# Performance work log

Measured on AMD Instinct MI355X. Metric: run time of the kernel, lower is better.

Reference implementation:

```python
import jax, jax.numpy as jnp
import numpy as np

VOCAB = 100000
EMBED = 300
HIDDEN = 300
BATCH = 32768
K_NEG = 10
N_CLASSES = 2
EPS = 1e-5
DENO_W = 1.0
CONO_W = 1.0


def setup_inputs() -> dict:
    key = jax.random.key(0)
    ks = jax.random.split(key, 12)
    init_range = 1.0 / EMBED
    return {
        "center_word_ids": jax.random.randint(ks[0], (BATCH,), 0, VOCAB),
        "context_word_ids": jax.random.randint(ks[1], (BATCH,), 0, VOCAB),
        "neg_context_ids": jax.random.randint(ks[2], (BATCH, K_NEG), 0, VOCAB),
        "party_label": jax.random.randint(ks[3], (BATCH,), 0, N_CLASSES),
        "center_emb": jax.random.uniform(ks[4], (VOCAB, EMBED), jnp.float32, -init_range, init_range),
        "context_emb": jax.random.normal(ks[5], (VOCAB, EMBED), jnp.float32) * 0.02,
        "W_enc": jax.random.normal(ks[6], (HIDDEN, EMBED), jnp.float32) * (1.0 / np.sqrt(EMBED)),
        "b_enc": jnp.zeros((HIDDEN,), jnp.float32),
        "W_dec": jax.random.normal(ks[7], (EMBED, HIDDEN), jnp.float32) * (1.0 / np.sqrt(HIDDEN)),
        "b_dec": jnp.zeros((EMBED,), jnp.float32),
        "W_cls": jax.random.normal(ks[8], (N_CLASSES, HIDDEN), jnp.float32) * (1.0 / np.sqrt(HIDDEN)),
        "b_cls": jnp.zeros((N_CLASSES,), jnp.float32),
    }


def reference(center_word_ids, context_word_ids, neg_context_ids, party_label,
              center_emb, context_emb, W_enc, b_enc, W_dec, b_dec, W_cls, b_cls):
    # encoder_forward (dropout p=0 -> identity)
    emb = center_emb[center_word_ids]                      # [B, E]
    enc = emb @ W_enc.T + b_enc                            # [B, H]
    # deno_forward: skip-gram negative sampling
    center_v = enc @ W_dec.T + b_dec                       # [B, E]
    ctx_v = context_emb[context_word_ids]                  # [B, E]
    pos_score = jnp.clip(jnp.sum(center_v * ctx_v, axis=1), -10.0, 10.0)
    pos = -jax.nn.log_sigmoid(pos_score)                   # [B]
    neg_v = context_emb[neg_context_ids]                   # [B, K, E]
    neg_score = jnp.clip(jnp.einsum('bke,be->bk', neg_v, center_v), -10.0, 10.0)
    neg = -jnp.sum(jax.nn.log_sigmoid(-neg_score), axis=1)  # [B]
    deno_loss = jnp.clip(jnp.mean(pos + neg), EPS, 10.0)
    # cono_forward + cross entropy
    logits = enc @ W_cls.T + b_cls                         # [B, C]
    logp = jax.nn.log_softmax(logits, axis=-1)
    nll = -jnp.take_along_axis(logp, party_label[:, None], axis=1)[:, 0]
    cono_loss = jnp.clip(jnp.mean(nll), EPS, 10.0)
    encoder_loss = jnp.clip(DENO_W * deno_loss + CONO_W * cono_loss, EPS, None)
    return jnp.stack([encoder_loss, deno_loss, cono_loss])
```

## Files before the change

### kernel.cpp

```cpp
#include <hip/hip_runtime.h>
#include <math.h>

#define VOCAB   100000
#define EMBED   300
#define HIDDEN  300
#define BATCH   32768
#define K_NEG   10
#define EPSV    1e-5f

#define KPAD      320
#define NPAD      384
#define CV_STRIDE 304
#define CTX8_STRIDE 304
#define FP8_SCALE 64.0f
#define FP8_DESCALE 0.015625f
#define NBUCKET 512

typedef __attribute__((ext_vector_type(8))) short  short8;
typedef __attribute__((ext_vector_type(4))) float  f32x4;
typedef __attribute__((ext_vector_type(2))) float  floatx2;

#if defined(__has_builtin)
#if __has_builtin(__builtin_amdgcn_cvt_pk_f32_fp8) && __has_builtin(__builtin_amdgcn_cvt_pk_fp8_f32)
#define HAVE_CVT_FP8 1
#endif
#endif

__device__ inline float b2f(unsigned short u) {
    union { unsigned int i; float f; } v; v.i = ((unsigned int)u) << 16; return v.f;
}
__device__ inline unsigned short f2b(float f) {
    union { float f; unsigned int i; } v; v.f = f;
    unsigned int r = v.i + 0x7FFFu + ((v.i >> 16) & 1u);
    return (unsigned short)(r >> 16);
}
__device__ inline void up2(unsigned int u, float& lo, float& hi) {
    union { unsigned int i; float f; } a, b;
    a.i = u << 16; b.i = u & 0xFFFF0000u;
    lo = a.f; hi = b.f;
}
__device__ inline float wave_red(float v) {
    #pragma unroll
    for (int o = 32; o; o >>= 1) v += __shfl_down(v, o);
    return v;
}
__device__ inline float softplusf(float x) {
    return x > 0.f ? x + log1pf(expf(-x)) : log1pf(expf(x));
}

__device__ inline float fp8_to_f(unsigned int u8) {
    const unsigned s = (u8 >> 7) & 1, e = (u8 >> 3) & 15, m = u8 & 7;
    float v;
    if (e) { union { unsigned i; float f; } b; b.i = ((e + 120u) << 23) | (m << 20); v = b.f; }
    else v = (float)m * 0.001953125f;
    return s ? -v : v;
}
__device__ inline unsigned char f_to_fp8(float x) {
    union { float f; unsigned i; } b; b.f = x;
    const unsigned s = (b.i >> 31) << 7;
    const float a = fabsf(x);
    if (a >= 440.f) return (unsigned char)(s | 0x7E);
    if (a < 0.015625f) {
        int m = (int)rintf(a * 512.f);
        return (unsigned char)(m >= 8 ? (s | 0x08) : (s | (unsigned)m));
    }
    unsigned r = (b.i & 0x7FFFFFFFu) + 0x7FFFFu + ((b.i >> 20) & 1u);
    unsigned e8 = (r >> 23) - 120u;
    unsigned m8 = (r >> 20) & 7u;
    if (e8 > 15u) return (unsigned char)(s | 0x7E);
    return (unsigned char)(s | (e8 << 3) | m8);
}
__device__ inline unsigned enc4fp8(float a, float b, float c, float d) {
#ifdef HAVE_CVT_FP8
    int v = 0;
    v = __builtin_amdgcn_cvt_pk_fp8_f32(a, b, v, false);
    v = __builtin_amdgcn_cvt_pk_fp8_f32(c, d, v, true);
    return (unsigned)v;
#else
    return (unsigned)f_to_fp8(a) | ((unsigned)f_to_fp8(b) << 8) |
           ((unsigned)f_to_fp8(c) << 16) | ((unsigned)f_to_fp8(d) << 24);
#endif
}
__device__ inline void dec4fp8(unsigned u, float* f) {
#ifdef HAVE_CVT_FP8
    floatx2 lo = __builtin_amdgcn_cvt_pk_f32_fp8((int)u, false);
    floatx2 hi = __builtin_amdgcn_cvt_pk_f32_fp8((int)u, true);
    f[0] = lo[0]; f[1] = lo[1]; f[2] = hi[0]; f[3] = hi[1];
#else
    f[0] = fp8_to_f(u); f[1] = fp8_to_f(u >> 8);
    f[2] = fp8_to_f(u >> 16); f[3] = fp8_to_f(u >> 24);
#endif
}

__device__ inline void load_lds16(const void* g, void* l) {
    __builtin_amdgcn_global_load_lds(
        (const __attribute__((address_space(1))) unsigned int*)g,
        (__attribute__((address_space(3))) unsigned int*)l, 16, 0, 0);
}

#define NW (2 * NPAD * 40)
#define NE (BATCH * 40)
#define NC (VOCAB * 19)

__global__ __launch_bounds__(256)
void prep_kernel(const float* __restrict__ W_enc, const float* __restrict__ W_dec,
                 const float* __restrict__ cemb, const int* __restrict__ cids,
                 const float* __restrict__ xemb,
                 unsigned short* __restrict__ wenc_b, unsigned short* __restrict__ wdec_b,
                 unsigned short* __restrict__ emb_b, unsigned char* __restrict__ ctx8)
{
    const int gid = blockIdx.x * 256 + threadIdx.x;
    if (gid < NW) {
        const int mat = gid / (NPAD * 40);
        const int rem = gid - mat * (NPAD * 40);
        const int r   = rem / 40;
        const int c8  = (rem - r * 40) * 8;
        const float* src = mat ? W_dec : W_enc;
        unsigned short* dst = mat ? wdec_b : wenc_b;
        unsigned short t[8];
        #pragma unroll
        for (int j = 0; j < 8; ++j) {
            const int c = c8 + j;
            t[j] = (r < 300 && c < 300) ? f2b(src[r * 300 + c]) : (unsigned short)0;
        }
        *(uint4*)(dst + (size_t)r * KPAD + c8) = *(const uint4*)t;
    } else if (gid < NW + NE) {
        const int g2  = gid - NW;
        const int row = g2 / 40;
        const int c8  = (g2 - row * 40) * 8;
        const float* src = cemb + (size_t)cids[row] * 300;
        unsigned short t[8];
        if (c8 + 7 < 300) {
            float4 a = *(const float4*)(src + c8);
            float4 b = *(const float4*)(src + c8 + 4);
            t[0]=f2b(a.x); t[1]=f2b(a.y); t[2]=f2b(a.z); t[3]=f2b(a.w);
            t[4]=f2b(b.x); t[5]=f2b(b.y); t[6]=f2b(b.z); t[7]=f2b(b.w);
        } else {
            #pragma unroll
            for (int j = 0; j < 8; ++j) {
                const int c = c8 + j;
                t[j] = (c < 300) ? f2b(src[c]) : (unsigned short)0;
            }
        }
        *(uint4*)(emb_b + (size_t)row * KPAD + c8) = *(const uint4*)t;
    } else if (gid < NW + NE + NC) {
        const int g3  = gid - (NW + NE);
        const int row = g3 / 19;
        const int l   = g3 - row * 19;
        const int e0  = l * 16;
        const float* src = xemb + (size_t)row * 300 + e0;
        float v[16];
        #pragma unroll
        for (int q = 0; q < 4; ++q) {
            if (e0 + q * 4 + 3 < 300) {
                float4 a = *(const float4*)(src + q * 4);
                v[q*4+0]=a.x; v[q*4+1]=a.y; v[q*4+2]=a.z; v[q*4+3]=a.w;
            } else {
                #pragma unroll
                for (int j = 0; j < 4; ++j) {
                    const int e = e0 + q * 4 + j;
                    v[q*4+j] = (e < 300) ? src[q*4+j] : 0.f;
                }
            }
        }
        unsigned u[4];
        #pragma unroll
        for (int q = 0; q < 4; ++q)
            u[q] = enc4fp8(v[q*4]*FP8_SCALE, v[q*4+1]*FP8_SCALE,
                           v[q*4+2]*FP8_SCALE, v[q*4+3]*FP8_SCALE);
        *(uint4*)(ctx8 + (size_t)row * CTX8_STRIDE + e0) = make_uint4(u[0],u[1],u[2],u[3]);
    }
}

template <int OSTRIDE, bool PAD_ZERO>
__global__ __launch_bounds__(256)
void mfma_gemm_kernel(const unsigned short* __restrict__ A,
                      const unsigned short* __restrict__ B,
                      const float* __restrict__ bias,
                      unsigned short* __restrict__ C)
{
    __shared__ unsigned short As[128 * 32];
    __shared__ unsigned short Bs[128 * 32];

    const int tid  = threadIdx.x;
    const int wave = tid >> 6;
    const int lane = tid & 63;
    const int m0 = blockIdx.y * 128;
    const int n0 = blockIdx.x * 128;

    const int wr = (wave & 1) * 64;
    const int wc = (wave >> 1) * 64;
    const int fr = lane & 15;
    const int fq = lane >> 4;

    const unsigned short* gA[2];
    const unsigned short* gB[2];
    int ldsOff[2];
    #pragma unroll
    for (int inst = 0; inst < 2; ++inst) {
        const int t = wave * 2 + inst;
        const int r = (t << 4) + (lane >> 2);
        const int c = ((lane & 3) - r - (r >> 2)) & 3;
        gA[inst] = A + (size_t)(m0 + r) * KPAD + c * 8;
        gB[inst] = B + (size_t)(n0 + r) * KPAD + c * 8;
        ldsOff[inst] = t << 9;
    }

    int aoff[4], boff[4];
    #pragma unroll
    for (int i = 0; i < 4; ++i) {
        const int ra = wr + i * 16 + fr;
        aoff[i] = (ra << 5) + (((fq + ra + (ra >> 2)) & 3) << 3);
        const int rb = wc + i * 16 + fr;
        boff[i] = (rb << 5) + (((fq + rb + (rb >> 2)) & 3) << 3);
    }

    f32x4 acc[4][4] = {};

    for (int k0 = 0; k0 < KPAD; k0 += 32) {
        #pragma unroll
        for (int inst = 0; inst < 2; ++inst) {
            load_lds16(gA[inst] + k0, As + ldsOff[inst]);
            load_lds16(gB[inst] + k0, Bs + ldsOff[inst]);
        }
        __syncthreads();

        short8 af[4], bf[4];
        #pragma unroll
        for (int i = 0; i < 4; ++i) af[i] = *(const short8*)&As[aoff[i]];
        #pragma unroll
        for (int j = 0; j < 4; ++j) bf[j] = *(const short8*)&Bs[boff[j]];
        __syncthreads();

        #pragma unroll
        for (int i = 0; i < 4; ++i)
            #pragma unroll
            for (int j = 0; j < 4; ++j)
                acc[i][j] = __builtin_amdgcn_mfma_f32_16x16x32_bf16(
                    af[i], bf[j], acc[i][j], 0, 0, 0);
    }

    #pragma unroll
    for (int i = 0; i < 4; ++i) {
        #pragma unroll
        for (int r = 0; r < 4; ++r) {
            const int m = m0 + wr + i * 16 + fq * 4 + r;
            unsigned short* crow = C + (size_t)m * OSTRIDE;
            #pragma unroll
            for (int j = 0; j < 4; ++j) {
                const int n = n0 + wc + j * 16 + fr;
                if (n < 300) {
                    crow[n] = f2b(acc[i][j][r] + bias[n]);
                } else if (PAD_ZERO && n < OSTRIDE) {
                    crow[n] = 0;
                }
            }
        }
    }
}

__global__ __launch_bounds__(256)
void score_ce_kernel(const unsigned short* __restrict__ cvb,
                     const unsigned short* __restrict__ encb,
                     const unsigned char* __restrict__ ctx8,
                     const int* __restrict__ ctx_ids, const int* __restrict__ neg_ids,
                     const int* __restrict__ labels,
                     const float* __restrict__ W_cls, const float* __restrict__ b_cls,
                     float* __restrict__ db, float* __restrict__ cb)
{
    const int g    = threadIdx.x >> 6;
    const int lane = threadIdx.x & 63;
    const int row  = blockIdx.x;
    const bool act = lane < 19;

    __shared__ float blk[2];
    if (threadIdx.x < 2) blk[threadIdx.x] = 0.f;
    __syncthreads();

    const uint4 Z4 = make_uint4(0, 0, 0, 0);

    if (g < 3) {
        int ids[4]; int nsc; bool hasPos = false;
        const int b = row * K_NEG;
        if (g == 0) {
            hasPos = true; nsc = 4;
            ids[0] = ctx_ids[row];
            ids[1] = neg_ids[b+0]; ids[2] = neg_ids[b+1]; ids[3] = neg_ids[b+2];
        } else if (g == 1) {
            nsc = 4;
            ids[0] = neg_ids[b+3]; ids[1] = neg_ids[b+4];
            ids[2] = neg_ids[b+5]; ids[3] = neg_ids[b+6];
        } else {
            nsc = 3;
            ids[0] = neg_ids[b+7]; ids[1] = neg_ids[b+8];
            ids[2] = neg_ids[b+9]; ids[3] = neg_ids[b+9];
        }

        const char* cvp = (const char*)(cvb + (size_t)row * CV_STRIDE);
        uint4 c0 = act ? *(const uint4*)(cvp + lane * 32)      : Z4;
        uint4 c1 = act ? *(const uint4*)(cvp + lane * 32 + 16) : Z4;

        uint4 gv[4];
        #pragma unroll
        for (int j = 0; j < 4; ++j)
            gv[j] = act ? *(const uint4*)(ctx8 + (size_t)ids[j] * CTX8_STRIDE + lane * 16)
                        : Z4;

        float cvf[16];
        up2(c0.x, cvf[0], cvf[1]);  up2(c0.y, cvf[2], cvf[3]);
        up2(c0.z, cvf[4], cvf[5]);  up2(c0.w, cvf[6], cvf[7]);
        up2(c1.x, cvf[8], cvf[9]);  up2(c1.y, cvf[10], cvf[11]);
        up2(c1.z, cvf[12], cvf[13]);up2(c1.w, cvf[14], cvf[15]);

        float ds[4];
        #pragma unroll
        for (int j = 0; j < 4; ++j) {
            float gf[16];
            dec4fp8(gv[j].x, gf); dec4fp8(gv[j].y, gf + 4);
            dec4fp8(gv[j].z, gf + 8); dec4fp8(gv[j].w, gf + 12);
            float s = 0.f;
            #pragma unroll
            for (int e = 0; e < 16; ++e) s = fmaf(cvf[e], gf[e], s);
            ds[j] = s;
        }
        #pragma unroll
        for (int j = 0; j < 4; ++j) ds[j] = wave_red(ds[j]);

        if (lane == 0) {
            float local = 0.f;
            #pragma unroll
            for (int j = 0; j < 4; ++j) {
                if (j < nsc) {
                    float s = fminf(10.f, fmaxf(-10.f, ds[j] * FP8_DESCALE));
                    local += softplusf((hasPos && j == 0) ? -s : s);
                }
            }
            atomicAdd(&blk[0], local);
        }
    } else {
        const char* evp = (const char*)(encb + (size_t)row * KPAD);
        uint4 e0 = act ? *(const uint4*)(evp + lane * 32)      : Z4;
        uint4 e1 = act ? *(const uint4*)(evp + lane * 32 + 16) : Z4;
        float ev[16];
        up2(e0.x, ev[0], ev[1]);  up2(e0.y, ev[2], ev[3]);
        up2(e0.z, ev[4], ev[5]);  up2(e0.w, ev[6], ev[7]);
        up2(e1.x, ev[8], ev[9]);  up2(e1.y, ev[10], ev[11]);
        up2(e1.z, ev[12], ev[13]);up2(e1.w, ev[14], ev[15]);

        float p0 = 0.f, p1 = 0.f;
        #pragma unroll
        for (int q = 0; q < 4; ++q) {
            const int e = lane * 16 + q * 4;
            if (e + 3 < 300) {
                float4 w0 = *(const float4*)(W_cls + e);
                float4 w1 = *(const float4*)(W_cls + 300 + e);
                p0 = fmaf(ev[q*4], w0.x, p0); p0 = fmaf(ev[q*4+1], w0.y, p0);
                p0 = fmaf(ev[q*4+2], w0.z, p0); p0 = fmaf(ev[q*4+3], w0.w, p0);
                p1 = fmaf(ev[q*4], w1.x, p1); p1 = fmaf(ev[q*4+1], w1.y, p1);
                p1 = fmaf(ev[q*4+2], w1.z, p1); p1 = fmaf(ev[q*4+3], w1.w, p1);
            } else {
                #pragma unroll
                for (int j = 0; j < 4; ++j) {
                    if (e + j < 300) {
                        p0 = fmaf(ev[q*4+j], W_cls[e + j], p0);
                        p1 = fmaf(ev[q*4+j], W_cls[300 + e + j], p1);
                    }
                }
            }
        }
        p0 = wave_red(p0); p1 = wave_red(p1);
        if (lane == 0) {
            const float l0 = p0 + b_cls[0];
            const float l1 = p1 + b_cls[1];
            const float mx = fmaxf(l0, l1);
            const float lse = mx + logf(expf(l0 - mx) + expf(l1 - mx));
            blk[1] = lse - (labels[row] ? l1 : l0);
        }
    }
    __syncthreads();
    if (threadIdx.x == 0) atomicAdd(&db[blockIdx.x & (NBUCKET - 1)], blk[0]);
    if (threadIdx.x == 1) atomicAdd(&cb[blockIdx.x & (NBUCKET - 1)], blk[1]);
}

__global__ __launch_bounds__(256)
void finalize_kernel(const float* __restrict__ db, const float* __restrict__ cb,
                     float* __restrict__ out)
{
    const int t = threadIdx.x;
    float d = db[t] + db[t + 256];
    float c = cb[t] + cb[t + 256];
    d = wave_red(d); c = wave_red(c);
    __shared__ float sd[4], sc[4];
    if ((t & 63) == 0) { sd[t >> 6] = d; sc[t >> 6] = c; }
    __syncthreads();
    if (t == 0) {
        const float inv = 1.0f / (float)BATCH;
        float deno = (sd[0] + sd[1] + sd[2] + sd[3]) * inv;
        float cono = (sc[0] + sc[1] + sc[2] + sc[3]) * inv;
        deno = fminf(10.f, fmaxf(EPSV, deno));
        cono = fminf(10.f, fmaxf(EPSV, cono));
        out[0] = fmaxf(EPSV, deno + cono);
        out[1] = deno;
        out[2] = cono;
    }
}

extern "C" void kernel_launch(void* const* d_in, const int* in_sizes, int n_in,
                              void* d_out, int out_size, void* d_ws, size_t ws_size,
                              hipStream_t stream)
{
    const int*   cids  = (const int*)d_in[0];
    const int*   ctx   = (const int*)d_in[1];
    const int*   neg   = (const int*)d_in[2];
    const int*   lab   = (const int*)d_in[3];
    const float* cemb  = (const float*)d_in[4];
    const float* xemb  = (const float*)d_in[5];
    const float* W_enc = (const float*)d_in[6];
    const float* b_enc = (const float*)d_in[7];
    const float* W_dec = (const float*)d_in[8];
    const float* b_dec = (const float*)d_in[9];
    const float* W_cls = (const float*)d_in[10];
    const float* b_cls = (const float*)d_in[11];
    float* out = (float*)d_out;

    unsigned short* emb_b  = (unsigned short*)d_ws;
    unsigned short* wenc_b = emb_b  + (size_t)BATCH * KPAD;
    unsigned short* wdec_b = wenc_b + (size_t)NPAD * KPAD;
    unsigned short* enc_b  = wdec_b + (size_t)NPAD * KPAD;
    unsigned short* cv_b   = enc_b  + (size_t)BATCH * KPAD;
    unsigned char*  ctx8   = (unsigned char*)(cv_b + (size_t)BATCH * CV_STRIDE);
    float* buckets = (float*)(ctx8 + (size_t)VOCAB * CTX8_STRIDE);
    float* db = buckets;
    float* cb = buckets + NBUCKET;

    hipMemsetAsync(buckets, 0, 2 * NBUCKET * sizeof(float), stream);

    const int nprep = (NW + NE + NC + 255) / 256;
    prep_kernel<<<nprep, 256, 0, stream>>>(W_enc, W_dec, cemb, cids, xemb,
                                           wenc_b, wdec_b, emb_b, ctx8);

    dim3 ggrid(3, BATCH / 128);
    mfma_gemm_kernel<KPAD, true><<<ggrid, 256, 0, stream>>>(emb_b, wenc_b, b_enc, enc_b);
    mfma_gemm_kernel<CV_STRIDE, true><<<ggrid, 256, 0, stream>>>(enc_b, wdec_b, b_dec, cv_b);

    score_ce_kernel<<<BATCH, 256, 0, stream>>>(cv_b, enc_b, ctx8, ctx, neg, lab,
                                               W_cls, b_cls, db, cb);
    finalize_kernel<<<1, 256, 0, stream>>>(db, cb, out);
}
```

Before: 426.3 us.

## Fold encoder and decoder into one weight and split score/CE kernels

After: 422.6 us. About the same (-0.9%).

```diff
diff --git a/kernel.cpp b/kernel.cpp
--- a/kernel.cpp
+++ b/kernel.cpp
@@ -12,6 +12,7 @@
 #define NPAD      384
 #define CV_STRIDE 304
 #define CTX8_STRIDE 304
+#define WC2_STRIDE 304
 #define FP8_SCALE 64.0f
 #define FP8_DESCALE 0.015625f
 #define NBUCKET 512
@@ -38,11 +39,6 @@
     union { unsigned int i; float f; } a, b;
     a.i = u << 16; b.i = u & 0xFFFF0000u;
     lo = a.f; hi = b.f;
-}
-__device__ inline float wave_red(float v) {
-    #pragma unroll
-    for (int o = 32; o; o >>= 1) v += __shfl_down(v, o);
-    return v;
 }
 __device__ inline float softplusf(float x) {
     return x > 0.f ? x + log1pf(expf(-x)) : log1pf(expf(x));
@@ -98,36 +94,18 @@
         (__attribute__((address_space(3))) unsigned int*)l, 16, 0, 0);
 }
 
-#define NW (2 * NPAD * 40)
 #define NE (BATCH * 40)
 #define NC (VOCAB * 19)
 
 __global__ __launch_bounds__(256)
-void prep_kernel(const float* __restrict__ W_enc, const float* __restrict__ W_dec,
-                 const float* __restrict__ cemb, const int* __restrict__ cids,
+void prep_kernel(const float* __restrict__ cemb, const int* __restrict__ cids,
                  const float* __restrict__ xemb,
-                 unsigned short* __restrict__ wenc_b, unsigned short* __restrict__ wdec_b,
                  unsigned short* __restrict__ emb_b, unsigned char* __restrict__ ctx8)
 {
     const int gid = blockIdx.x * 256 + threadIdx.x;
-    if (gid < NW) {
-        const int mat = gid / (NPAD * 40);
-        const int rem = gid - mat * (NPAD * 40);
-        const int r   = rem / 40;
-        const int c8  = (rem - r * 40) * 8;
-        const float* src = mat ? W_dec : W_enc;
-        unsigned short* dst = mat ? wdec_b : wenc_b;
-        unsigned short t[8];
-        #pragma unroll
-        for (int j = 0; j < 8; ++j) {
-            const int c = c8 + j;
-            t[j] = (r < 300 && c < 300) ? f2b(src[r * 300 + c]) : (unsigned short)0;
-        }
-        *(uint4*)(dst + (size_t)r * KPAD + c8) = *(const uint4*)t;
-    } else if (gid < NW + NE) {
-        const int g2  = gid - NW;
-        const int row = g2 / 40;
-        const int c8  = (g2 - row * 40) * 8;
+    if (gid < NE) {
+        const int row = gid / 40;
+        const int c8  = (gid - row * 40) * 8;
         const float* src = cemb + (size_t)cids[row] * 300;
         unsigned short t[8];
         if (c8 + 7 < 300) {
@@ -143,8 +121,8 @@
             }
         }
         *(uint4*)(emb_b + (size_t)row * KPAD + c8) = *(const uint4*)t;
-    } else if (gid < NW + NE + NC) {
-        const int g3  = gid - (NW + NE);
+    } else if (gid < NE + NC) {
+        const int g3  = gid - NE;
         const int row = g3 / 19;
         const int l   = g3 - row * 19;
         const int e0  = l * 16;
@@ -172,15 +150,84 @@
     }
 }
 
-template <int OSTRIDE, bool PAD_ZERO>
 __global__ __launch_bounds__(256)
-void mfma_gemm_kernel(const unsigned short* __restrict__ A,
-                      const unsigned short* __restrict__ B,
-                      const float* __restrict__ bias,
-                      unsigned short* __restrict__ C)
-{
-    __shared__ unsigned short As[128 * 32];
-    __shared__ unsigned short Bs[128 * 32];
+void w2_kernel(const float* __restrict__ Wd, const float* __restrict__ We,
+               unsigned short* __restrict__ w2p)
+{
+    __shared__ float ds[16][33];
+    __shared__ float es[32][17];
+    const int tid = threadIdx.x;
+    const int tn = tid >> 4, tk = tid & 15;
+    const int n = blockIdx.y * 16 + tn;
+    const int k = blockIdx.x * 16 + tk;
+
+    float acc = 0.f;
+    for (int h0 = 0; h0 < 300; h0 += 32) {
+        {
+            const int i = tid * 2;
+            const int a = i >> 5, h = i & 31;
+            const int rr = blockIdx.y * 16 + a;
+            #pragma unroll
+            for (int j = 0; j < 2; ++j) {
+                const int hh = h + j;
+                ds[a][hh] = (rr < 300 && h0 + hh < 300) ? Wd[rr * 300 + h0 + hh] : 0.f;
+            }
+        }
+        {
+            const int i = tid * 2;
+            const int h = i >> 4, c = i & 15;
+            const int cc = blockIdx.x * 16 + c;
+            #pragma unroll
+            for (int j = 0; j < 2; ++j)
+                es[h][c + j] = (h0 + h < 300 && cc + j < 300) ? We[(h0 + h) * 300 + cc + j] : 0.f;
+        }
+        __syncthreads();
+        #pragma unroll
+        for (int h = 0; h < 32; ++h)
+            acc = fmaf(ds[tn][h], es[h][tk], acc);
+        __syncthreads();
+    }
+    if (n < NPAD && k < KPAD)
+        w2p[n * KPAD + k] = (n < 300 && k < 300) ? f2b(acc) : (unsigned short)0;
+}
+
+__global__ __launch_bounds__(320)
+void wb_kernel(const float* __restrict__ Wd, const float* __restrict__ We,
+               const float* __restrict__ Wc, const float* __restrict__ b_enc,
+               const float* __restrict__ b_dec, const float* __restrict__ b_cls,
+               float* __restrict__ wc2, float* __restrict__ bias2, float* __restrict__ bc2)
+{
+    const int c = threadIdx.x;
+    if (c < WC2_STRIDE) {
+        float b2 = 0.f, a0 = 0.f, a1 = 0.f;
+        if (c < 300) {
+            for (int k = 0; k < 300; ++k) b2 = fmaf(Wd[c * 300 + k], b_enc[k], b2);
+            for (int h = 0; h < 300; ++h) {
+                const float we = We[h * 300 + c];
+                a0 = fmaf(Wc[h], we, a0);
+                a1 = fmaf(Wc[300 + h], we, a1);
+            }
+            b2 += b_dec[c];
+        }
+        bias2[c] = b2;
+        wc2[c] = a0;
+        wc2[WC2_STRIDE + c] = a1;
+    } else if (c < WC2_STRIDE + 2) {
+        const int j = c - WC2_STRIDE;
+        float s = 0.f;
+        for (int h = 0; h < 300; ++h) s = fmaf(Wc[j * 300 + h], b_enc[h], s);
+        bc2[j] = s + b_cls[j];
+    }
+}
+
+__global__ __launch_bounds__(256)
+void gemm_cv_kernel(const unsigned short* __restrict__ A,
+                    const unsigned short* __restrict__ B,
+                    const float* __restrict__ bias,
+                    unsigned short* __restrict__ C)
+{
+    __shared__ unsigned short As[2][128 * 32];
+    __shared__ unsigned short Bs[2][128 * 32];
 
     const int tid  = threadIdx.x;
     const int wave = tid >> 6;
@@ -217,27 +264,35 @@
 
     f32x4 acc[4][4] = {};
 
-    for (int k0 = 0; k0 < KPAD; k0 += 32) {
-        #pragma unroll
-        for (int inst = 0; inst < 2; ++inst) {
-            load_lds16(gA[inst] + k0, As + ldsOff[inst]);
-            load_lds16(gB[inst] + k0, Bs + ldsOff[inst]);
-        }
+    #pragma unroll
+    for (int inst = 0; inst < 2; ++inst) {
+        load_lds16(gA[inst], &As[0][ldsOff[inst]]);
+        load_lds16(gB[inst], &Bs[0][ldsOff[inst]]);
+    }
+
+    int cur = 0;
+    for (int ki = 0; ki < KPAD / 32; ++ki) {
         __syncthreads();
-
+        if (ki + 1 < KPAD / 32) {
+            const int k0 = (ki + 1) * 32;
+            #pragma unroll
+            for (int inst = 0; inst < 2; ++inst) {
+                load_lds16(gA[inst] + k0, &As[cur ^ 1][ldsOff[inst]]);
+                load_lds16(gB[inst] + k0, &Bs[cur ^ 1][ldsOff[inst]]);
+            }
+        }
         short8 af[4], bf[4];
         #pragma unroll
-        for (int i = 0; i < 4; ++i) af[i] = *(const short8*)&As[aoff[i]];
-        #pragma unroll
-        for (int j = 0; j < 4; ++j) bf[j] = *(const short8*)&Bs[boff[j]];
-        __syncthreads();
-
+        for (int i = 0; i < 4; ++i) af[i] = *(const short8*)&As[cur][aoff[i]];
+        #pragma unroll
+        for (int j = 0; j < 4; ++j) bf[j] = *(const short8*)&Bs[cur][boff[j]];
         #pragma unroll
         for (int i = 0; i < 4; ++i)
             #pragma unroll
             for (int j = 0; j < 4; ++j)
                 acc[i][j] = __builtin_amdgcn_mfma_f32_16x16x32_bf16(
                     af[i], bf[j], acc[i][j], 0, 0, 0);
+        cur ^= 1;
     }
 
     #pragma unroll
@@ -245,13 +300,13 @@
         #pragma unroll
         for (int r = 0; r < 4; ++r) {
             const int m = m0 + wr + i * 16 + fq * 4 + r;
-            unsigned short* crow = C + (size_t)m * OSTRIDE;
+            unsigned short* crow = C + (size_t)m * CV_STRIDE;
             #pragma unroll
             for (int j = 0; j < 4; ++j) {
                 const int n = n0 + wc + j * 16 + fr;
                 if (n < 300) {
                     crow[n] = f2b(acc[i][j][r] + bias[n]);
-                } else if (PAD_ZERO && n < OSTRIDE) {
+                } else if (n < CV_STRIDE) {
                     crow[n] = 0;
                 }
             }
@@ -260,128 +315,131 @@
 }
 
 __global__ __launch_bounds__(256)
-void score_ce_kernel(const unsigned short* __restrict__ cvb,
-                     const unsigned short* __restrict__ encb,
-                     const unsigned char* __restrict__ ctx8,
-                     const int* __restrict__ ctx_ids, const int* __restrict__ neg_ids,
-                     const int* __restrict__ labels,
-                     const float* __restrict__ W_cls, const float* __restrict__ b_cls,
-                     float* __restrict__ db, float* __restrict__ cb)
-{
-    const int g    = threadIdx.x >> 6;
+void score_kernel(const unsigned short* __restrict__ cvb,
+                  const unsigned char* __restrict__ ctx8,
+                  const int* __restrict__ ctx_ids, const int* __restrict__ neg_ids,
+                  float* __restrict__ db)
+{
+    const int wid  = threadIdx.x >> 6;
     const int lane = threadIdx.x & 63;
-    const int row  = blockIdx.x;
-    const bool act = lane < 19;
-
-    __shared__ float blk[2];
-    if (threadIdx.x < 2) blk[threadIdx.x] = 0.f;
-    __syncthreads();
+    const int l5   = lane & 31;
+    const int unit = blockIdx.x * 8 + wid * 2 + (lane >> 5);
+    const int row  = unit / 3;
+    const int g    = unit - row * 3;
+    const bool act = l5 < 19;
+
+    const int b = row * K_NEG;
+    int ids[4]; bool inc[4]; bool pos[4];
+    #pragma unroll
+    for (int j = 0; j < 4; ++j) {
+        const int t = g * 4 - 1 + j;
+        pos[j] = (t < 0);
+        inc[j] = (t <= 9);
+        ids[j] = pos[j] ? ctx_ids[row] : neg_ids[b + (t > 9 ? 9 : t)];
+    }
 
     const uint4 Z4 = make_uint4(0, 0, 0, 0);
-
-    if (g < 3) {
-        int ids[4]; int nsc; bool hasPos = false;
-        const int b = row * K_NEG;
-        if (g == 0) {
-            hasPos = true; nsc = 4;
-            ids[0] = ctx_ids[row];
-            ids[1] = neg_ids[b+0]; ids[2] = neg_ids[b+1]; ids[3] = neg_ids[b+2];
-        } else if (g == 1) {
-            nsc = 4;
-            ids[0] = neg_ids[b+3]; ids[1] = neg_ids[b+4];
-            ids[2] = neg_ids[b+5]; ids[3] = neg_ids[b+6];
-        } else {
-            nsc = 3;
-            ids[0] = neg_ids[b+7]; ids[1] = neg_ids[b+8];
-            ids[2] = neg_ids[b+9]; ids[3] = neg_ids[b+9];
-        }
-
-        const char* cvp = (const char*)(cvb + (size_t)row * CV_STRIDE);
-        uint4 c0 = act ? *(const uint4*)(cvp + lane * 32)      : Z4;
-        uint4 c1 = act ? *(const uint4*)(cvp + lane * 32 + 16) : Z4;
-
-        uint4 gv[4];
-        #pragma unroll
-        for (int j = 0; j < 4; ++j)
-            gv[j] = act ? *(const uint4*)(ctx8 + (size_t)ids[j] * CTX8_STRIDE + lane * 16)
-                        : Z4;
-
-        float cvf[16];
-        up2(c0.x, cvf[0], cvf[1]);  up2(c0.y, cvf[2], cvf[3]);
-        up2(c0.z, cvf[4], cvf[5]);  up2(c0.w, cvf[6], cvf[7]);
-        up2(c1.x, cvf[8], cvf[9]);  up2(c1.y, cvf[10], cvf[11]);
-        up2(c1.z, cvf[12], cvf[13]);up2(c1.w, cvf[14], cvf[15]);
-
-        float ds[4];
+    const char* cvp = (const char*)(cvb + (size_t)row * CV_STRIDE);
+    uint4 c0 = act ? *(const uint4*)(cvp + l5 * 32)      : Z4;
+    uint4 c1 = act ? *(const uint4*)(cvp + l5 * 32 + 16) : Z4;
+
+    uint4 gv[4];
+    #pragma unroll
+    for (int j = 0; j < 4; ++j)
+        gv[j] = act ? *(const uint4*)(ctx8 + (size_t)ids[j] * CTX8_STRIDE + l5 * 16) : Z4;
+
+    float cvf[16];
+    up2(c0.x, cvf[0], cvf[1]);  up2(c0.y, cvf[2], cvf[3]);
+    up2(c0.z, cvf[4], cvf[5]);  up2(c0.w, cvf[6], cvf[7]);
+    up2(c1.x, cvf[8], cvf[9]);  up2(c1.y, cvf[10], cvf[11]);
+    up2(c1.z, cvf[12], cvf[13]);up2(c1.w, cvf[14], cvf[15]);
+
+    float ds[4];
+    #pragma unroll
+    for (int j = 0; j < 4; ++j) {
+        float gf[16];
+        dec4fp8(gv[j].x, gf); dec4fp8(gv[j].y, gf + 4);
+        dec4fp8(gv[j].z, gf + 8); dec4fp8(gv[j].w, gf + 12);
+        float s = 0.f;
+        #pragma unroll
+        for (int e = 0; e < 16; ++e) s = fmaf(cvf[e], gf[e], s);
+        ds[j] = s;
+    }
+    #pragma unroll
+    for (int j = 0; j < 4; ++j) {
+        float v = ds[j];
+        #pragma unroll
+        for (int m = 16; m; m >>= 1) v += __shfl_xor(v, m);
+        ds[j] = v;
+    }
+
+    if (l5 == 0) {
+        float local = 0.f;
         #pragma unroll
         for (int j = 0; j < 4; ++j) {
-            float gf[16];
-            dec4fp8(gv[j].x, gf); dec4fp8(gv[j].y, gf + 4);
-            dec4fp8(gv[j].z, gf + 8); dec4fp8(gv[j].w, gf + 12);
-            float s = 0.f;
-            #pragma unroll
-            for (int e = 0; e < 16; ++e) s = fmaf(cvf[e], gf[e], s);
-            ds[j] = s;
-        }
-        #pragma unroll
-        for (int j = 0; j < 4; ++j) ds[j] = wave_red(ds[j]);
-
-        if (lane == 0) {
-            float local = 0.f;
-            #pragma unroll
-            for (int j = 0; j < 4; ++j) {
-                if (j < nsc) {
-                    float s = fminf(10.f, fmaxf(-10.f, ds[j] * FP8_DESCALE));
-                    local += softplusf((hasPos && j == 0) ? -s : s);
-                }
-            }
-            atomicAdd(&blk[0], local);
-        }
-    } else {
-        const char* evp = (const char*)(encb + (size_t)row * KPAD);
-        uint4 e0 = act ? *(const uint4*)(evp + lane * 32)      : Z4;
-        uint4 e1 = act ? *(const uint4*)(evp + lane * 32 + 16) : Z4;
-        float ev[16];
-        up2(e0.x, ev[0], ev[1]);  up2(e0.y, ev[2], ev[3]);
-        up2(e0.z, ev[4], ev[5]);  up2(e0.w, ev[6], ev[7]);
-        up2(e1.x, ev[8], ev[9]);  up2(e1.y, ev[10], ev[11]);
-        up2(e1.z, ev[12], ev[13]);up2(e1.w, ev[14], ev[15]);
-
-        float p0 = 0.f, p1 = 0.f;
+            if (inc[j]) {
+                float s = fminf(10.f, fmaxf(-10.f, ds[j] * FP8_DESCALE));
+                local += softplusf(pos[j] ? -s : s);
+            }
+        }
+        atomicAdd(&db[blockIdx.x & (NBUCKET - 1)], local);
+    }
+}
+
+__global__ __launch_bounds__(256)
+void ce_kernel(const unsigned short* __restrict__ embb,
+               const int* __restrict__ labels,
+               const float* __restrict__ wc2, const float* __restrict__ bc2,
+               float* __restrict__ cb)
+{
+    const int wid  = threadIdx.x >> 6;
+    const int lane = threadIdx.x & 63;
+    const int l5   = lane & 31;
+    const int row  = blockIdx.x * 8 + wid * 2 + (lane >> 5);
+    const bool act = l5 < 19;
+
+    const uint4 Z4 = make_uint4(0, 0, 0, 0);
+    const char* evp = (const char*)(embb + (size_t)row * KPAD);
+    uint4 e0 = act ? *(const uint4*)(evp + l5 * 32)      : Z4;
+    uint4 e1 = act ? *(const uint4*)(evp + l5 * 32 + 16) : Z4;
+    float ev[16];
+    up2(e0.x, ev[0], ev[1]);  up2(e0.y, ev[2], ev[3]);
+    up2(e0.z, ev[4], ev[5]);  up2(e0.w, ev[6], ev[7]);
+    up2(e1.x, ev[8], ev[9]);  up2(e1.y, ev[10], ev[11]);
+    up2(e1.z, ev[12], ev[13]);up2(e1.w, ev[14], ev[15]);
+
+    float p0 = 0.f, p1 = 0.f;
+    if (act) {
+        const float* w0 = wc2 + l5 * 16;
+        const float* w1 = wc2 + WC2_STRIDE + l5 * 16;
         #pragma unroll
         for (int q = 0; q < 4; ++q) {
-            const int e = lane * 16 + q * 4;
-            if (e + 3 < 300) {
-                float4 w0 = *(const float4*)(W_cls + e);
-                float4 w1 = *(const float4*)(W_cls + 300 + e);
-                p0 = fmaf(ev[q*4], w0.x, p0); p0 = fmaf(ev[q*4+1], w0.y, p0);
-                p0 = fmaf(ev[q*4+2], w0.z, p0); p0 = fmaf(ev[q*4+3], w0.w, p0);
-                p1 = fmaf(ev[q*4], w1.x, p1); p1 = fmaf(ev[q*4+1], w1.y, p1);
-                p1 = fmaf(ev[q*4+2], w1.z, p1); p1 = fmaf(ev[q*4+3], w1.w, p1);
-            } else {
-                #pragma unroll
-                for (int j = 0; j < 4; ++j) {
-                    if (e + j < 300) {
-                        p0 = fmaf(ev[q*4+j], W_cls[e + j], p0);
-                        p1 = fmaf(ev[q*4+j], W_cls[300 + e + j], p1);
-                    }
-                }
-            }
-        }
-        p0 = wave_red(p0); p1 = wave_red(p1);
-        if (lane == 0) {
-            const float l0 = p0 + b_cls[0];
-            const float l1 = p1 + b_cls[1];
-            const float mx = fmaxf(l0, l1);
-            const float lse = mx + logf(expf(l0 - mx) + expf(l1 - mx));
-            blk[1] = lse - (labels[row] ? l1 : l0);
-        }
-    }
-    __syncthreads();
-    if (threadIdx.x == 0) atomicAdd(&db[blockIdx.x & (NBUCKET - 1)], blk[0]);
-    if (threadIdx.x == 1) atomicAdd(&cb[blockIdx.x & (NBUCKET - 1)], blk[1]);
-}
-
+            float4 a = *(const float4*)(w0 + q * 4);
+            float4 c = *(const float4*)(w1 + q * 4);
+            p0 = fmaf(ev[q*4], a.x, p0); p0 = fmaf(ev[q*4+1], a.y, p0);
+            p0 = fmaf(ev[q*4+2], a.z, p0); p0 = fmaf(ev[q*4+3], a.w, p0);
+            p1 = fmaf(ev[q*4], c.x, p1); p1 = fmaf(ev[q*4+1], c.y, p1);
+            p1 = fmaf(ev[q*4+2], c.z, p1); p1 = fmaf(ev[q*4+3], c.w, p1);
+        }
+    }
+    #pragma unroll
+    for (int m = 16; m; m >>= 1) { p0 += __shfl_xor(p0, m); p1 += __shfl_xor(p1, m); }
+
+    if (l5 == 0) {
+        const float l0 = p0 + bc2[0];
+        const float l1 = p1 + bc2[1];
+        const float mx = fmaxf(l0, l1);
+        const float lse = mx + logf(expf(l0 - mx) + expf(l1 - mx));
+        const float nll = lse - (labels[row] ? l1 : l0);
+        atomicAdd(&cb[blockIdx.x & (NBUCKET - 1)], nll);
+    }
+}
+
+__device__ inline float wave_red64(float v) {
+    #pragma unroll
+    for (int o = 32; o; o >>= 1) v += __shfl_down(v, o);
+    return v;
+}
 __global__ __launch_bounds__(256)
 void finalize_kernel(const float* __restrict__ db, const float* __restrict__ cb,
                      float* __restrict__ out)
@@ -389,7 +447,7 @@
     const int t = threadIdx.x;
     float d = db[t] + db[t + 256];
     float c = cb[t] + cb[t + 256];
-    d = wave_red(d); c = wave_red(c);
+    d = wave_red64(d); c = wave_red64(c);
     __shared__ float sd[4], sc[4];
     if ((t & 63) == 0) { sd[t >> 6] = d; sc[t >> 6] = c; }
     __syncthreads();
@@ -423,27 +481,30 @@
     const float* b_cls = (const float*)d_in[11];
     float* out = (float*)d_out;
 
-    unsigned short* emb_b  = (unsigned short*)d_ws;
-    unsigned short* wenc_b = emb_b  + (size_t)BATCH * KPAD;
-    unsigned short* wdec_b = wenc_b + (size_t)NPAD * KPAD;
-    unsigned short* enc_b  = wdec_b + (size_t)NPAD * KPAD;
-    unsigned short* cv_b   = enc_b  + (size_t)BATCH * KPAD;
-    unsigned char*  ctx8   = (unsigned char*)(cv_b + (size_t)BATCH * CV_STRIDE);
-    float* buckets = (float*)(ctx8 + (size_t)VOCAB * CTX8_STRIDE);
-    float* db = buckets;
-    float* cb = buckets + NBUCKET;
-
-    hipMemsetAsync(buckets, 0, 2 * NBUCKET * sizeof(float), stream);
-
-    const int nprep = (NW + NE + NC + 255) / 256;
-    prep_kernel<<<nprep, 256, 0, stream>>>(W_enc, W_dec, cemb, cids, xemb,
-                                           wenc_b, wdec_b, emb_b, ctx8);
+    unsigned short* emb_b = (unsigned short*)d_ws;
+    unsigned short* cv_b  = emb_b + (size_t)BATCH * KPAD;
+    unsigned char*  ctx8  = (unsigned char*)(cv_b + (size_t)BATCH * CV_STRIDE);
+    unsigned short* w2p   = (unsigned short*)(ctx8 + (size_t)VOCAB * CTX8_STRIDE);
+    float* wc2   = (float*)(w2p + (size_t)NPAD * KPAD);
+    float* bias2 = wc2 + 2 * WC2_STRIDE;
+    float* bc2   = bias2 + WC2_STRIDE;
+    float* db    = bc2 + 4;
+    float* cb    = db + NBUCKET;
+
+    hipMemsetAsync(db, 0, 2 * NBUCKET * sizeof(float), stream);
+
+    prep_kernel<<<(NE + NC + 255) / 256, 256, 0, stream>>>(cemb, cids, xemb, emb_b, ctx8);
+
+    dim3 wgrid(KPAD / 16, NPAD / 16);
+    w2_kernel<<<wgrid, 256, 0, stream>>>(W_dec, W_enc, w2p);
+    wb_kernel<<<1, 320, 0, stream>>>(W_dec, W_enc, W_cls, b_enc, b_dec, b_cls,
+                                     wc2, bias2, bc2);
 
     dim3 ggrid(3, BATCH / 128);
-    mfma_gemm_kernel<KPAD, true><<<ggrid, 256, 0, stream>>>(emb_b, wenc_b, b_enc, enc_b);
-    mfma_gemm_kernel<CV_STRIDE, true><<<ggrid, 256, 0, stream>>>(enc_b, wdec_b, b_dec, cv_b);
-
-    score_ce_kernel<<<BATCH, 256, 0, stream>>>(cv_b, enc_b, ctx8, ctx, neg, lab,
-                                               W_cls, b_cls, db, cb);
+    gemm_cv_kernel<<<ggrid, 256, 0, stream>>>(emb_b, w2p, bias2, cv_b);
+
+    score_kernel<<<3 * BATCH / 8, 256, 0, stream>>>(cv_b, ctx8, ctx, neg, db);
+    ce_kernel<<<BATCH / 8, 256, 0, stream>>>(emb_b, lab, wc2, bc2, cb);
+
     finalize_kernel<<<1, 256, 0, stream>>>(db, cb, out);
 }
```
